# Performance work log

Hardware: AMD Instinct MI355X
Metric: run time of the kernel (lower is better)

The kernel has to match this reference:

```python
import jax, jax.numpy as jnp
import numpy as np

D = 2048
N_SLOTS = 8
ALPHA_MIN = 0.02
FAST_DECAY = 0.95
ALPHA_BOOST = 1.0
B = 16384


def setup_inputs() -> dict:
    key = jax.random.key(0)
    ks = jax.random.split(key, 12)
    h = jax.random.normal(ks[0], (B, D), dtype=jnp.float32)
    neighbor_msg = jax.random.normal(ks[1], (B, D), dtype=jnp.float32)
    keys = jax.random.normal(ks[2], (N_SLOTS, D), dtype=jnp.float32) / (D ** 0.5)
    # torch nn.Linear convention: W [out, in], y = x @ W.T + b
    Wr = jax.random.normal(ks[3], (D, D), dtype=jnp.float32) * 0.02
    br = jnp.zeros((D,), dtype=jnp.float32)
    Wc = jax.random.normal(ks[4], (2, 2 * D), dtype=jnp.float32) * 0.02
    bc = jnp.zeros((2,), dtype=jnp.float32)
    Ww = jax.random.normal(ks[5], (D, 2 * D), dtype=jnp.float32) * 0.02
    bw = jnp.zeros((D,), dtype=jnp.float32)
    state = jax.random.normal(ks[6], (N_SLOTS, D), dtype=jnp.float32) * 0.1
    fast = jax.random.normal(ks[7], (N_SLOTS, D), dtype=jnp.float32) * 0.1
    return {"h": h, "neighbor_msg": neighbor_msg, "keys": keys,
            "Wr": Wr, "br": br, "Wc": Wc, "bc": bc, "Ww": Ww, "bw": bw,
            "state": state, "fast": fast}


def reference(h, neighbor_msg, keys, Wr, br, Wc, bc, Ww, bw, state, fast):
    # read_proj
    q = h @ Wr.T + br                                  # [B, D]
    attn = jax.nn.softmax(q @ keys.T, axis=-1)         # [B, n_slots]
    read = attn @ (state + fast)                       # [B, D]
    # ctrl -> add/erase gates (erase computed but unused downstream, as in source)
    ctrl = jnp.concatenate([h, read], axis=-1) @ Wc.T + bc   # [B, 2]
    add = jax.nn.sigmoid(ctrl[:, 0:1])
    erase = jax.nn.sigmoid(ctrl[:, 1:2])
    alpha = jnp.clip(ALPHA_MIN + (1.0 - ALPHA_MIN) * jnp.mean(add), 0.0, 1.0)
    alpha = jnp.clip(alpha * ALPHA_BOOST, 0.0, 1.0)
    # attention-weighted write into slots
    w_in = jnp.concatenate([h + neighbor_msg, read], axis=-1)  # [B, 2D]
    delta = attn.T @ (w_in @ Ww.T + bw)                # [n_slots, D]
    new_state = (1.0 - alpha) * state + alpha * delta
    new_fast = FAST_DECAY * fast + (1.0 - FAST_DECAY) * delta
    return read, attn, alpha, new_state, new_fast
```

## Files before the change

### kernel.cpp

```cpp
#include <hip/hip_runtime.h>
#include <math.h>

#define D 2048
#define NS 8
#define BTOT 16384

#define ATTN_OFF  ((size_t)BTOT * D)
#define ALPHA_OFF (ATTN_OFF + (size_t)BTOT * NS)
#define STATE_OFF (ALPHA_OFF + 1)
#define FAST_OFF  (STATE_OFF + (size_t)NS * D)

#define WS_SM    0
#define WS_KPX   16384
#define WS_GS    34816
#define WS_PB    51200
#define WS_LOG   67584
#define WS_LB    215040
#define WS_SWC   215048
#define WS_GALL  215056
#define WS_ALPHA 215136

__global__ void __launch_bounds__(256) kZ(const float* __restrict__ st, const float* __restrict__ fa,
                                          const float* __restrict__ Wc, float* __restrict__ ws) {
  int i = blockIdx.x * 256 + threadIdx.x;
  if (i < 16384) {
    ws[WS_SM + i] = st[i] + fa[i];
  } else if (i < 32768) {
    ws[WS_KPX + (i - 16384)] = 0.f;
  } else if (i < 34816) {
    ws[WS_KPX + 16384 + (i - 32768)] = Wc[i - 32768];
  } else if (i < 51200) {
    ws[WS_PB + (i - 34816)] = 0.f;
  } else if (i < 198656) {
    ws[WS_LOG + (i - 51200)] = 0.f;
  } else if (i < 198736) {
    ws[WS_GALL + (i - 198656)] = 0.f;
  }
}

__global__ void __launch_bounds__(256) kA(const float* __restrict__ keys,
                                          const float* __restrict__ Wr,
                                          float* __restrict__ kpx) {
  int e = blockIdx.x * 256 + threadIdx.x;
  int d0 = blockIdx.y * 128;
  float acc[NS] = {0.f,0.f,0.f,0.f,0.f,0.f,0.f,0.f};
  for (int d = d0; d < d0 + 128; ++d) {
    float wv = Wr[(size_t)d * D + e];
#pragma unroll
    for (int s = 0; s < NS; ++s) acc[s] += keys[s * D + d] * wv;
  }
#pragma unroll
  for (int s = 0; s < NS; ++s) atomicAdd(&kpx[s * D + e], acc[s]);
}

__global__ void __launch_bounds__(256) kC(const float* __restrict__ keys,
                                          const float* __restrict__ br,
                                          const float* __restrict__ Wc,
                                          const float* __restrict__ sm,
                                          float* __restrict__ lb, float* __restrict__ swc) {
  int t = threadIdx.x;
  float aL[NS] = {0.f,0.f,0.f,0.f,0.f,0.f,0.f,0.f};
  float aS[NS] = {0.f,0.f,0.f,0.f,0.f,0.f,0.f,0.f};
  for (int idx = t; idx < D; idx += 256) {
    float brv = br[idx];
    float wcr = Wc[D + idx];
#pragma unroll
    for (int s = 0; s < NS; ++s) {
      aL[s] += keys[s * D + idx] * brv;
      aS[s] += sm[s * D + idx] * wcr;
    }
  }
#pragma unroll
  for (int off = 32; off > 0; off >>= 1) {
#pragma unroll
    for (int s = 0; s < NS; ++s) {
      aL[s] += __shfl_down(aL[s], off);
      aS[s] += __shfl_down(aS[s], off);
    }
  }
  __shared__ float red[4 * 16];
  int lane = t & 63, wid = t >> 6;
  if (lane == 0) {
#pragma unroll
    for (int s = 0; s < NS; ++s) { red[wid * 16 + s] = aL[s]; red[wid * 16 + 8 + s] = aS[s]; }
  }
  __syncthreads();
  if (t < 16) {
    float v = red[t] + red[16 + t] + red[32 + t] + red[48 + t];
    if (t < 8) lb[t] = v; else swc[t - 8] = v;
  }
}

__global__ void __launch_bounds__(256) k1a(const float* __restrict__ h,
                                           const float* __restrict__ kpx,
                                           float* __restrict__ logits) {
  __shared__ float lds[4][64 * 65];
  int t = threadIdx.x;
  int w = t >> 6, lane = t & 63;
  int wave_id = blockIdx.x * 4 + w;
  int rg = wave_id >> 3, chunk = wave_id & 7;
  int rowbase = rg * 64, colbase = chunk * 256;
  float acc[9] = {0.f,0.f,0.f,0.f,0.f,0.f,0.f,0.f,0.f};
  int c16 = lane & 15, rq = lane >> 4;
  for (int sub = 0; sub < 4; ++sub) {
    int cb = colbase + sub * 64;
#pragma unroll
    for (int i = 0; i < 16; ++i) {
      int r = i * 4 + rq;
      float4 v = *(const float4*)(h + (size_t)(rowbase + r) * D + cb + c16 * 4);
      float* dst = &lds[w][r * 65 + c16 * 4];
      dst[0] = v.x; dst[1] = v.y; dst[2] = v.z; dst[3] = v.w;
    }
    __syncthreads();
    const float* hr = &lds[w][lane * 65];
#pragma unroll
    for (int j4 = 0; j4 < 16; ++j4) {
      float h0 = hr[j4 * 4 + 0], h1 = hr[j4 * 4 + 1], h2 = hr[j4 * 4 + 2], h3 = hr[j4 * 4 + 3];
#pragma unroll
      for (int s = 0; s < 9; ++s) {
        const float* kr = kpx + s * D + cb + j4 * 4;
        acc[s] += h0 * kr[0] + h1 * kr[1] + h2 * kr[2] + h3 * kr[3];
      }
    }
    __syncthreads();
  }
#pragma unroll
  for (int s = 0; s < 9; ++s) atomicAdd(&logits[(size_t)(rowbase + lane) * 9 + s], acc[s]);
}

__global__ void __launch_bounds__(256) k1b(const float* __restrict__ logits,
                                           const float* __restrict__ lb, const float* __restrict__ swc,
                                           const float* __restrict__ bc,
                                           float* __restrict__ attn, float* __restrict__ gall) {
  int t = threadIdx.x;
  int b = blockIdx.x * 256 + t;
  const float* lrow = logits + (size_t)b * 9;
  float lg[NS]; float m = -1e30f;
#pragma unroll
  for (int s = 0; s < NS; ++s) { lg[s] = lrow[s] + lb[s]; m = fmaxf(m, lg[s]); }
  float av[NS]; float sum = 0.f;
#pragma unroll
  for (int s = 0; s < NS; ++s) { av[s] = expf(lg[s] - m); sum += av[s]; }
  float inv = 1.f / sum;
  float* ao = attn + (size_t)b * NS;
#pragma unroll
  for (int s = 0; s < NS; ++s) { av[s] *= inv; ao[s] = av[s]; }
  float x = lrow[8] + bc[0];
#pragma unroll
  for (int s = 0; s < NS; ++s) x += av[s] * swc[s];
  float add = 1.f / (1.f + expf(-x));
  float v[73];
#pragma unroll
  for (int i = 0; i < NS; ++i)
#pragma unroll
    for (int j = 0; j < NS; ++j) v[i * 8 + j] = av[i] * av[j];
#pragma unroll
  for (int s = 0; s < NS; ++s) v[64 + s] = av[s];
  v[72] = add;
#pragma unroll
  for (int off = 32; off > 0; off >>= 1) {
#pragma unroll
    for (int k = 0; k < 73; ++k) v[k] += __shfl_down(v[k], off);
  }
  __shared__ float red[4 * 73];
  int lane = t & 63, wid = t >> 6;
  if (lane == 0) {
#pragma unroll
    for (int k = 0; k < 73; ++k) red[wid * 73 + k] = v[k];
  }
  __syncthreads();
  if (t < 73) {
    float tot = red[t] + red[73 + t] + red[146 + t] + red[219 + t];
    atomicAdd(&gall[t], tot);
  }
}

static __device__ __forceinline__ float4 f4fma(float s, float4 a, float4 c) {
  c.x += s * a.x; c.y += s * a.y; c.z += s * a.z; c.w += s * a.w; return c;
}

__global__ void __launch_bounds__(256) k2n(const float* __restrict__ h, const float* __restrict__ nm,
                                           const float* __restrict__ sm, const float* __restrict__ attn,
                                           float* __restrict__ readout, float* __restrict__ pb) {
  __shared__ float4 lp[4][NS][64];
  int t = threadIdx.x;
  int c4 = t & 63, r4 = t >> 6;
  int chunk = blockIdx.x, rc = blockIdx.y;
  int fbase = chunk * 64 + c4;
  const float4* sm4 = (const float4*)sm;
  float4 S[NS];
#pragma unroll
  for (int s = 0; s < NS; ++s) S[s] = sm4[s * 512 + fbase];
  float4 P[NS];
#pragma unroll
  for (int s = 0; s < NS; ++s) P[s] = make_float4(0.f, 0.f, 0.f, 0.f);
  int rowbase = rc * 256;
  for (int it = 0; it < 64; ++it) {
    int row = rowbase + it * 4 + r4;
    float4 hv = ((const float4*)h)[(size_t)row * 512 + fbase];
    float4 nv = ((const float4*)nm)[(size_t)row * 512 + fbase];
    const float* ar = attn + (size_t)row * NS;
    float4 w = make_float4(hv.x + nv.x, hv.y + nv.y, hv.z + nv.z, hv.w + nv.w);
    float4 rd = make_float4(0.f, 0.f, 0.f, 0.f);
#pragma unroll
    for (int s = 0; s < NS; ++s) {
      float a = ar[s];
      rd = f4fma(a, S[s], rd);
      P[s] = f4fma(a, w, P[s]);
    }
    ((float4*)readout)[(size_t)row * 512 + fbase] = rd;
  }
#pragma unroll
  for (int s = 0; s < NS; ++s) lp[r4][s][c4] = P[s];
  __syncthreads();
  for (int k = t; k < 512; k += 256) {
    int s = k >> 6, c = k & 63;
    float4 a = lp[0][s][c], b = lp[1][s][c], cc = lp[2][s][c], d = lp[3][s][c];
    float4 v = make_float4(a.x + b.x + cc.x + d.x, a.y + b.y + cc.y + d.y,
                           a.z + b.z + cc.z + d.z, a.w + b.w + cc.w + d.w);
    float* dst = pb + s * D + chunk * 256 + c * 4;
    atomicAdd(dst + 0, v.x); atomicAdd(dst + 1, v.y);
    atomicAdd(dst + 2, v.z); atomicAdd(dst + 3, v.w);
  }
}

__global__ void k3n(const float* __restrict__ gall, const float* __restrict__ sm,
                    float* __restrict__ gs, float* __restrict__ alphap, float* __restrict__ alphaout) {
  int i = blockIdx.x * 256 + threadIdx.x;
  int s = i >> 11, e = i & 2047;
  float sum = 0.f;
#pragma unroll
  for (int sp = 0; sp < NS; ++sp) sum += gall[s * 8 + sp] * sm[sp * D + e];
  gs[i] = sum;
  if (i == 0) {
    float mean = gall[72] * (1.f / (float)BTOT);
    float al = 0.02f + 0.98f * mean;
    al = fminf(fmaxf(al, 0.f), 1.f);
    alphap[0] = al;
    alphaout[0] = al;
  }
}

__global__ void __launch_bounds__(256) k4(const float* __restrict__ Ww, const float* __restrict__ bw,
                                          const float* __restrict__ st, const float* __restrict__ fa,
                                          const float* __restrict__ p, const float* __restrict__ gs,
                                          const float* __restrict__ cs, const float* __restrict__ alphap,
                                          float* __restrict__ outst, float* __restrict__ outfa) {
  int dd = blockIdx.x, t = threadIdx.x;
  const float4* wr = (const float4*)(Ww + (size_t)dd * (2 * D));
  float4 w0 = wr[t], w1 = wr[256 + t], w2 = wr[512 + t], w3 = wr[768 + t];
  const float4* p4 = (const float4*)p;
  const float4* g4 = (const float4*)gs;
  float acc[NS];
#pragma unroll
  for (int s = 0; s < NS; ++s) {
    float4 pa = p4[s * 512 + t], pb2 = p4[s * 512 + 256 + t];
    float4 ga = g4[s * 512 + t], gb = g4[s * 512 + 256 + t];
    acc[s] = w0.x * pa.x + w0.y * pa.y + w0.z * pa.z + w0.w * pa.w
           + w1.x * pb2.x + w1.y * pb2.y + w1.z * pb2.z + w1.w * pb2.w
           + w2.x * ga.x + w2.y * ga.y + w2.z * ga.z + w2.w * ga.w
           + w3.x * gb.x + w3.y * gb.y + w3.z * gb.z + w3.w * gb.w;
  }
#pragma unroll
  for (int off = 32; off > 0; off >>= 1) {
#pragma unroll
    for (int v = 0; v < NS; ++v) acc[v] += __shfl_down(acc[v], off);
  }
  __shared__ float red[32];
  int lane = t & 63, wid = t >> 6;
  if (lane == 0) {
#pragma unroll
    for (int v = 0; v < NS; ++v) red[wid * 8 + v] = acc[v];
  }
  __syncthreads();
  if (t < NS) {
    float tot = red[t] + red[8 + t] + red[16 + t] + red[24 + t];
    float delta = tot + cs[t] * bw[dd];
    float al = alphap[0];
    size_t idx = (size_t)t * D + dd;
    outst[idx] = (1.f - al) * st[idx] + al * delta;
    outfa[idx] = 0.95f * fa[idx] + 0.05f * delta;
  }
}

extern "C" void kernel_launch(void* const* d_in, const int* in_sizes, int n_in,
                              void* d_out, int out_size, void* d_ws, size_t ws_size,
                              hipStream_t stream) {
  const float* h    = (const float*)d_in[0];
  const float* nm   = (const float*)d_in[1];
  const float* keys = (const float*)d_in[2];
  const float* Wr   = (const float*)d_in[3];
  const float* br   = (const float*)d_in[4];
  const float* Wc   = (const float*)d_in[5];
  const float* bc   = (const float*)d_in[6];
  const float* Ww   = (const float*)d_in[7];
  const float* bw   = (const float*)d_in[8];
  const float* st   = (const float*)d_in[9];
  const float* fa   = (const float*)d_in[10];
  float* out = (float*)d_out;
  float* ws  = (float*)d_ws;

  float* sm     = ws + WS_SM;
  float* kpx    = ws + WS_KPX;
  float* gsb    = ws + WS_GS;
  float* pb     = ws + WS_PB;
  float* logits = ws + WS_LOG;
  float* lb     = ws + WS_LB;
  float* swc    = ws + WS_SWC;
  float* gall   = ws + WS_GALL;
  float* alphap = ws + WS_ALPHA;
  float* attn   = out + ATTN_OFF;

  kZ<<<777, 256, 0, stream>>>(st, fa, Wc, ws);
  kA<<<dim3(8, 16), 256, 0, stream>>>(keys, Wr, kpx);
  kC<<<1, 256, 0, stream>>>(keys, br, Wc, sm, lb, swc);
  k1a<<<512, 256, 0, stream>>>(h, kpx, logits);
  k1b<<<64, 256, 0, stream>>>(logits, lb, swc, bc, attn, gall);
  k2n<<<dim3(8, 64), 256, 0, stream>>>(h, nm, sm, attn, out, pb);
  k3n<<<64, 256, 0, stream>>>(gall, sm, gsb, alphap, out + ALPHA_OFF);
  k4<<<2048, 256, 0, stream>>>(Ww, bw, st, fa, pb, gsb, gall + 64, alphap, out + STATE_OFF, out + FAST_OFF);
}
```

Measured before the change: 513.8 us.

## Fuse logits with softmax and gate, accumulate attn-weighted read in k2n

Merges the h·kpx logits kernel and the softmax/gate kernel into one kernel. It keeps the projected keys in LDS and reduces each row within a wave, so the logits workspace and its atomics go away. The Gram-matrix path (attn^T attn then k3n) is replaced by accumulating attn^T·read directly inside k2n. Alpha is now computed in k4, k3n is dropped, and kA, kC and k2n get finer grids. The cost is extra float atomics on gsb from k2n and more registers there, with occupancy capped by launch bounds.

```diff
diff --git a/kernel.cpp b/kernel.cpp
--- a/kernel.cpp
+++ b/kernel.cpp
@@ -14,11 +14,9 @@
 #define WS_KPX   16384
 #define WS_GS    34816
 #define WS_PB    51200
-#define WS_LOG   67584
 #define WS_LB    215040
 #define WS_SWC   215048
 #define WS_GALL  215056
-#define WS_ALPHA 215136
 
 __global__ void __launch_bounds__(256) kZ(const float* __restrict__ st, const float* __restrict__ fa,
                                           const float* __restrict__ Wc, float* __restrict__ ws) {
@@ -30,11 +28,11 @@
   } else if (i < 34816) {
     ws[WS_KPX + 16384 + (i - 32768)] = Wc[i - 32768];
   } else if (i < 51200) {
-    ws[WS_PB + (i - 34816)] = 0.f;
-  } else if (i < 198656) {
-    ws[WS_LOG + (i - 51200)] = 0.f;
-  } else if (i < 198736) {
-    ws[WS_GALL + (i - 198656)] = 0.f;
+    ws[WS_GS + (i - 34816)] = 0.f;
+  } else if (i < 67584) {
+    ws[WS_PB + (i - 51200)] = 0.f;
+  } else if (i < 67680) {
+    ws[WS_LB + (i - 67584)] = 0.f;
   }
 }
 
@@ -42,9 +40,9 @@
                                           const float* __restrict__ Wr,
                                           float* __restrict__ kpx) {
   int e = blockIdx.x * 256 + threadIdx.x;
-  int d0 = blockIdx.y * 128;
+  int d0 = blockIdx.y * 64;
   float acc[NS] = {0.f,0.f,0.f,0.f,0.f,0.f,0.f,0.f};
-  for (int d = d0; d < d0 + 128; ++d) {
+  for (int d = d0; d < d0 + 64; ++d) {
     float wv = Wr[(size_t)d * D + e];
 #pragma unroll
     for (int s = 0; s < NS; ++s) acc[s] += keys[s * D + d] * wv;
@@ -59,119 +57,99 @@
                                           const float* __restrict__ sm,
                                           float* __restrict__ lb, float* __restrict__ swc) {
   int t = threadIdx.x;
-  float aL[NS] = {0.f,0.f,0.f,0.f,0.f,0.f,0.f,0.f};
-  float aS[NS] = {0.f,0.f,0.f,0.f,0.f,0.f,0.f,0.f};
-  for (int idx = t; idx < D; idx += 256) {
-    float brv = br[idx];
-    float wcr = Wc[D + idx];
-#pragma unroll
-    for (int s = 0; s < NS; ++s) {
-      aL[s] += keys[s * D + idx] * brv;
-      aS[s] += sm[s * D + idx] * wcr;
-    }
+  int idx = blockIdx.x * 256 + t;
+  float brv = br[idx];
+  float wcr = Wc[D + idx];
+  float v[16];
+#pragma unroll
+  for (int s = 0; s < NS; ++s) {
+    v[s]     = keys[s * D + idx] * brv;
+    v[8 + s] = sm[s * D + idx] * wcr;
   }
 #pragma unroll
   for (int off = 32; off > 0; off >>= 1) {
 #pragma unroll
-    for (int s = 0; s < NS; ++s) {
-      aL[s] += __shfl_down(aL[s], off);
-      aS[s] += __shfl_down(aS[s], off);
-    }
+    for (int k = 0; k < 16; ++k) v[k] += __shfl_down(v[k], off);
   }
   __shared__ float red[4 * 16];
   int lane = t & 63, wid = t >> 6;
   if (lane == 0) {
 #pragma unroll
-    for (int s = 0; s < NS; ++s) { red[wid * 16 + s] = aL[s]; red[wid * 16 + 8 + s] = aS[s]; }
+    for (int k = 0; k < 16; ++k) red[wid * 16 + k] = v[k];
   }
   __syncthreads();
   if (t < 16) {
-    float v = red[t] + red[16 + t] + red[32 + t] + red[48 + t];
-    if (t < 8) lb[t] = v; else swc[t - 8] = v;
-  }
-}
-
-__global__ void __launch_bounds__(256) k1a(const float* __restrict__ h,
-                                           const float* __restrict__ kpx,
-                                           float* __restrict__ logits) {
-  __shared__ float lds[4][64 * 65];
+    float tot = red[t] + red[16 + t] + red[32 + t] + red[48 + t];
+    if (t < 8) atomicAdd(&lb[t], tot); else atomicAdd(&swc[t - 8], tot);
+  }
+}
+
+__global__ void __launch_bounds__(256) k1aF(const float* __restrict__ h,
+                                            const float* __restrict__ kpx,
+                                            const float* __restrict__ lb, const float* __restrict__ swc,
+                                            const float* __restrict__ bc,
+                                            float* __restrict__ attn, float* __restrict__ gall) {
+  __shared__ float4 kl[9 * 512];
+  __shared__ float red2[4 * 9];
   int t = threadIdx.x;
+  const float4* kp4 = (const float4*)kpx;
+  for (int i = t; i < 4608; i += 256) kl[i] = kp4[i];
+  __syncthreads();
+
   int w = t >> 6, lane = t & 63;
-  int wave_id = blockIdx.x * 4 + w;
-  int rg = wave_id >> 3, chunk = wave_id & 7;
-  int rowbase = rg * 64, colbase = chunk * 256;
-  float acc[9] = {0.f,0.f,0.f,0.f,0.f,0.f,0.f,0.f,0.f};
-  int c16 = lane & 15, rq = lane >> 4;
-  for (int sub = 0; sub < 4; ++sub) {
-    int cb = colbase + sub * 64;
-#pragma unroll
-    for (int i = 0; i < 16; ++i) {
-      int r = i * 4 + rq;
-      float4 v = *(const float4*)(h + (size_t)(rowbase + r) * D + cb + c16 * 4);
-      float* dst = &lds[w][r * 65 + c16 * 4];
-      dst[0] = v.x; dst[1] = v.y; dst[2] = v.z; dst[3] = v.w;
-    }
-    __syncthreads();
-    const float* hr = &lds[w][lane * 65];
-#pragma unroll
-    for (int j4 = 0; j4 < 16; ++j4) {
-      float h0 = hr[j4 * 4 + 0], h1 = hr[j4 * 4 + 1], h2 = hr[j4 * 4 + 2], h3 = hr[j4 * 4 + 3];
+  int row0 = blockIdx.x * 32 + w * 8;
+  float lbv[8], swv[8];
+#pragma unroll
+  for (int s = 0; s < NS; ++s) { lbv[s] = lb[s]; swv[s] = swc[s]; }
+  float bc0 = bc[0];
+  float cs[9] = {0.f,0.f,0.f,0.f,0.f,0.f,0.f,0.f,0.f};
+
+  for (int r = 0; r < 8; ++r) {
+    int row = row0 + r;
+    const float4* h4 = (const float4*)h + (size_t)row * 512;
+    float4 hv[8];
+#pragma unroll
+    for (int j = 0; j < 8; ++j) hv[j] = h4[lane + 64 * j];
+    float acc[9] = {0.f,0.f,0.f,0.f,0.f,0.f,0.f,0.f,0.f};
+#pragma unroll
+    for (int j = 0; j < 8; ++j) {
 #pragma unroll
       for (int s = 0; s < 9; ++s) {
-        const float* kr = kpx + s * D + cb + j4 * 4;
-        acc[s] += h0 * kr[0] + h1 * kr[1] + h2 * kr[2] + h3 * kr[3];
+        float4 kv = kl[s * 512 + lane + 64 * j];
+        acc[s] += hv[j].x * kv.x + hv[j].y * kv.y + hv[j].z * kv.z + hv[j].w * kv.w;
       }
     }
-    __syncthreads();
-  }
-#pragma unroll
-  for (int s = 0; s < 9; ++s) atomicAdd(&logits[(size_t)(rowbase + lane) * 9 + s], acc[s]);
-}
-
-__global__ void __launch_bounds__(256) k1b(const float* __restrict__ logits,
-                                           const float* __restrict__ lb, const float* __restrict__ swc,
-                                           const float* __restrict__ bc,
-                                           float* __restrict__ attn, float* __restrict__ gall) {
-  int t = threadIdx.x;
-  int b = blockIdx.x * 256 + t;
-  const float* lrow = logits + (size_t)b * 9;
-  float lg[NS]; float m = -1e30f;
-#pragma unroll
-  for (int s = 0; s < NS; ++s) { lg[s] = lrow[s] + lb[s]; m = fmaxf(m, lg[s]); }
-  float av[NS]; float sum = 0.f;
-#pragma unroll
-  for (int s = 0; s < NS; ++s) { av[s] = expf(lg[s] - m); sum += av[s]; }
-  float inv = 1.f / sum;
-  float* ao = attn + (size_t)b * NS;
-#pragma unroll
-  for (int s = 0; s < NS; ++s) { av[s] *= inv; ao[s] = av[s]; }
-  float x = lrow[8] + bc[0];
-#pragma unroll
-  for (int s = 0; s < NS; ++s) x += av[s] * swc[s];
-  float add = 1.f / (1.f + expf(-x));
-  float v[73];
-#pragma unroll
-  for (int i = 0; i < NS; ++i)
-#pragma unroll
-    for (int j = 0; j < NS; ++j) v[i * 8 + j] = av[i] * av[j];
-#pragma unroll
-  for (int s = 0; s < NS; ++s) v[64 + s] = av[s];
-  v[72] = add;
-#pragma unroll
-  for (int off = 32; off > 0; off >>= 1) {
-#pragma unroll
-    for (int k = 0; k < 73; ++k) v[k] += __shfl_down(v[k], off);
-  }
-  __shared__ float red[4 * 73];
-  int lane = t & 63, wid = t >> 6;
+#pragma unroll
+    for (int off = 32; off > 0; off >>= 1) {
+#pragma unroll
+      for (int s = 0; s < 9; ++s) acc[s] += __shfl_xor(acc[s], off);
+    }
+    float lg[8]; float m = -1e30f;
+#pragma unroll
+    for (int s = 0; s < NS; ++s) { lg[s] = acc[s] + lbv[s]; m = fmaxf(m, lg[s]); }
+    float sum = 0.f;
+#pragma unroll
+    for (int s = 0; s < NS; ++s) { lg[s] = expf(lg[s] - m); sum += lg[s]; }
+    float inv = 1.f / sum;
+    float x = acc[8] + bc0;
+#pragma unroll
+    for (int s = 0; s < NS; ++s) { lg[s] *= inv; x += lg[s] * swv[s]; cs[s] += lg[s]; }
+    float add = 1.f / (1.f + expf(-x));
+    cs[8] += add;
+    if (lane == 0) {
+      float4* ao = (float4*)(attn + (size_t)row * NS);
+      ao[0] = make_float4(lg[0], lg[1], lg[2], lg[3]);
+      ao[1] = make_float4(lg[4], lg[5], lg[6], lg[7]);
+    }
+  }
   if (lane == 0) {
 #pragma unroll
-    for (int k = 0; k < 73; ++k) red[wid * 73 + k] = v[k];
-  }
-  __syncthreads();
-  if (t < 73) {
-    float tot = red[t] + red[73 + t] + red[146 + t] + red[219 + t];
-    atomicAdd(&gall[t], tot);
+    for (int k = 0; k < 9; ++k) red2[w * 9 + k] = cs[k];
+  }
+  __syncthreads();
+  if (t < 9) {
+    float tot = red2[t] + red2[9 + t] + red2[18 + t] + red2[27 + t];
+    atomicAdd(&gall[64 + t], tot);
   }
 }
 
@@ -179,9 +157,10 @@
   c.x += s * a.x; c.y += s * a.y; c.z += s * a.z; c.w += s * a.w; return c;
 }
 
-__global__ void __launch_bounds__(256) k2n(const float* __restrict__ h, const float* __restrict__ nm,
-                                           const float* __restrict__ sm, const float* __restrict__ attn,
-                                           float* __restrict__ readout, float* __restrict__ pb) {
+__global__ void __launch_bounds__(256, 3) k2n(const float* __restrict__ h, const float* __restrict__ nm,
+                                              const float* __restrict__ sm, const float* __restrict__ attn,
+                                              float* __restrict__ readout, float* __restrict__ pb,
+                                              float* __restrict__ gsb) {
   __shared__ float4 lp[4][NS][64];
   int t = threadIdx.x;
   int c4 = t & 63, r4 = t >> 6;
@@ -191,23 +170,27 @@
   float4 S[NS];
 #pragma unroll
   for (int s = 0; s < NS; ++s) S[s] = sm4[s * 512 + fbase];
-  float4 P[NS];
-#pragma unroll
-  for (int s = 0; s < NS; ++s) P[s] = make_float4(0.f, 0.f, 0.f, 0.f);
-  int rowbase = rc * 256;
-  for (int it = 0; it < 64; ++it) {
+  float4 P[NS], Q[NS];
+#pragma unroll
+  for (int s = 0; s < NS; ++s) { P[s] = make_float4(0.f,0.f,0.f,0.f); Q[s] = make_float4(0.f,0.f,0.f,0.f); }
+  int rowbase = rc * 128;
+  for (int it = 0; it < 32; ++it) {
     int row = rowbase + it * 4 + r4;
     float4 hv = ((const float4*)h)[(size_t)row * 512 + fbase];
     float4 nv = ((const float4*)nm)[(size_t)row * 512 + fbase];
     const float* ar = attn + (size_t)row * NS;
-    float4 w = make_float4(hv.x + nv.x, hv.y + nv.y, hv.z + nv.z, hv.w + nv.w);
+    float a[NS];
+#pragma unroll
+    for (int s = 0; s < NS; ++s) a[s] = ar[s];
+    float4 wv = make_float4(hv.x + nv.x, hv.y + nv.y, hv.z + nv.z, hv.w + nv.w);
     float4 rd = make_float4(0.f, 0.f, 0.f, 0.f);
 #pragma unroll
     for (int s = 0; s < NS; ++s) {
-      float a = ar[s];
-      rd = f4fma(a, S[s], rd);
-      P[s] = f4fma(a, w, P[s]);
+      rd = f4fma(a[s], S[s], rd);
+      P[s] = f4fma(a[s], wv, P[s]);
     }
+#pragma unroll
+    for (int s = 0; s < NS; ++s) Q[s] = f4fma(a[s], rd, Q[s]);
     ((float4*)readout)[(size_t)row * 512 + fbase] = rd;
   }
 #pragma unroll
@@ -215,37 +198,34 @@
   __syncthreads();
   for (int k = t; k < 512; k += 256) {
     int s = k >> 6, c = k & 63;
-    float4 a = lp[0][s][c], b = lp[1][s][c], cc = lp[2][s][c], d = lp[3][s][c];
-    float4 v = make_float4(a.x + b.x + cc.x + d.x, a.y + b.y + cc.y + d.y,
-                           a.z + b.z + cc.z + d.z, a.w + b.w + cc.w + d.w);
+    float4 a0 = lp[0][s][c], b0 = lp[1][s][c], c0 = lp[2][s][c], d0 = lp[3][s][c];
+    float4 v = make_float4(a0.x + b0.x + c0.x + d0.x, a0.y + b0.y + c0.y + d0.y,
+                           a0.z + b0.z + c0.z + d0.z, a0.w + b0.w + c0.w + d0.w);
     float* dst = pb + s * D + chunk * 256 + c * 4;
     atomicAdd(dst + 0, v.x); atomicAdd(dst + 1, v.y);
     atomicAdd(dst + 2, v.z); atomicAdd(dst + 3, v.w);
   }
-}
-
-__global__ void k3n(const float* __restrict__ gall, const float* __restrict__ sm,
-                    float* __restrict__ gs, float* __restrict__ alphap, float* __restrict__ alphaout) {
-  int i = blockIdx.x * 256 + threadIdx.x;
-  int s = i >> 11, e = i & 2047;
-  float sum = 0.f;
-#pragma unroll
-  for (int sp = 0; sp < NS; ++sp) sum += gall[s * 8 + sp] * sm[sp * D + e];
-  gs[i] = sum;
-  if (i == 0) {
-    float mean = gall[72] * (1.f / (float)BTOT);
-    float al = 0.02f + 0.98f * mean;
-    al = fminf(fmaxf(al, 0.f), 1.f);
-    alphap[0] = al;
-    alphaout[0] = al;
+  __syncthreads();
+#pragma unroll
+  for (int s = 0; s < NS; ++s) lp[r4][s][c4] = Q[s];
+  __syncthreads();
+  for (int k = t; k < 512; k += 256) {
+    int s = k >> 6, c = k & 63;
+    float4 a0 = lp[0][s][c], b0 = lp[1][s][c], c0 = lp[2][s][c], d0 = lp[3][s][c];
+    float4 v = make_float4(a0.x + b0.x + c0.x + d0.x, a0.y + b0.y + c0.y + d0.y,
+                           a0.z + b0.z + c0.z + d0.z, a0.w + b0.w + c0.w + d0.w);
+    float* dst = gsb + s * D + chunk * 256 + c * 4;
+    atomicAdd(dst + 0, v.x); atomicAdd(dst + 1, v.y);
+    atomicAdd(dst + 2, v.z); atomicAdd(dst + 3, v.w);
   }
 }
 
 __global__ void __launch_bounds__(256) k4(const float* __restrict__ Ww, const float* __restrict__ bw,
                                           const float* __restrict__ st, const float* __restrict__ fa,
                                           const float* __restrict__ p, const float* __restrict__ gs,
-                                          const float* __restrict__ cs, const float* __restrict__ alphap,
-                                          float* __restrict__ outst, float* __restrict__ outfa) {
+                                          const float* __restrict__ gall,
+                                          float* __restrict__ outst, float* __restrict__ outfa,
+                                          float* __restrict__ alphaout) {
   int dd = blockIdx.x, t = threadIdx.x;
   const float4* wr = (const float4*)(Ww + (size_t)dd * (2 * D));
   float4 w0 = wr[t], w1 = wr[256 + t], w2 = wr[512 + t], w3 = wr[768 + t];
@@ -275,11 +255,16 @@
   __syncthreads();
   if (t < NS) {
     float tot = red[t] + red[8 + t] + red[16 + t] + red[24 + t];
-    float delta = tot + cs[t] * bw[dd];
-    float al = alphap[0];
+    float delta = tot + gall[64 + t] * bw[dd];
+    float al = 0.02f + 0.98f * (gall[72] * (1.f / (float)BTOT));
+    al = fminf(fmaxf(al, 0.f), 1.f);
     size_t idx = (size_t)t * D + dd;
     outst[idx] = (1.f - al) * st[idx] + al * delta;
     outfa[idx] = 0.95f * fa[idx] + 0.05f * delta;
+  }
+  if (dd == 0 && t == 0) {
+    float al = 0.02f + 0.98f * (gall[72] * (1.f / (float)BTOT));
+    alphaout[0] = fminf(fmaxf(al, 0.f), 1.f);
   }
 }
 
@@ -300,23 +285,20 @@
   float* out = (float*)d_out;
   float* ws  = (float*)d_ws;
 
-  float* sm     = ws + WS_SM;
-  float* kpx    = ws + WS_KPX;
-  float* gsb    = ws + WS_GS;
-  float* pb     = ws + WS_PB;
-  float* logits = ws + WS_LOG;
-  float* lb     = ws + WS_LB;
-  float* swc    = ws + WS_SWC;
-  float* gall   = ws + WS_GALL;
-  float* alphap = ws + WS_ALPHA;
-  float* attn   = out + ATTN_OFF;
-
-  kZ<<<777, 256, 0, stream>>>(st, fa, Wc, ws);
-  kA<<<dim3(8, 16), 256, 0, stream>>>(keys, Wr, kpx);
-  kC<<<1, 256, 0, stream>>>(keys, br, Wc, sm, lb, swc);
-  k1a<<<512, 256, 0, stream>>>(h, kpx, logits);
-  k1b<<<64, 256, 0, stream>>>(logits, lb, swc, bc, attn, gall);
-  k2n<<<dim3(8, 64), 256, 0, stream>>>(h, nm, sm, attn, out, pb);
-  k3n<<<64, 256, 0, stream>>>(gall, sm, gsb, alphap, out + ALPHA_OFF);
-  k4<<<2048, 256, 0, stream>>>(Ww, bw, st, fa, pb, gsb, gall + 64, alphap, out + STATE_OFF, out + FAST_OFF);
-}
+  float* sm   = ws + WS_SM;
+  float* kpx  = ws + WS_KPX;
+  float* gsb  = ws + WS_GS;
+  float* pb   = ws + WS_PB;
+  float* lb   = ws + WS_LB;
+  float* swc  = ws + WS_SWC;
+  float* gall = ws + WS_GALL;
+  float* attn = out + ATTN_OFF;
+
+  kZ<<<265, 256, 0, stream>>>(st, fa, Wc, ws);
+  kA<<<dim3(8, 32), 256, 0, stream>>>(keys, Wr, kpx);
+  kC<<<8, 256, 0, stream>>>(keys, br, Wc, sm, lb, swc);
+  k1aF<<<512, 256, 0, stream>>>(h, kpx, lb, swc, bc, attn, gall);
+  k2n<<<dim3(8, 128), 256, 0, stream>>>(h, nm, sm, attn, out, pb, gsb);
+  k4<<<2048, 256, 0, stream>>>(Ww, bw, st, fa, pb, gsb, gall, out + STATE_OFF, out + FAST_OFF,
+                               out + ALPHA_OFF);
+}
```

Measured after the change: 503.1 us. 1.02x faster.
